# Optimization experiments

Hardware: AMD Instinct MI355X
Metric: run time of the kernel (lower is better)

The kernel has to match this reference:

```python
import jax, jax.numpy as jnp
import numpy as np

N = 100000
E = 1600000
F_IN = 512
H1, C1 = 8, 8          # conv1: 8 heads x 8 channels, concat -> 64
H2, C2 = 1, 16         # conv2: 1 head x num_classes=16, mean
NEG_SLOPE = 0.2


def setup_inputs() -> dict:
    key = jax.random.key(0)
    ks = jax.random.split(key, 10)
    x = jax.random.normal(ks[0], (N, F_IN), dtype=jnp.float32)
    edge_index = jax.random.randint(ks[1], (2, E), 0, N, dtype=jnp.int64)
    s1 = 1.0 / np.sqrt(F_IN)
    s2 = 1.0 / np.sqrt(H1 * C1)
    W1 = jax.random.normal(ks[2], (F_IN, H1 * C1), dtype=jnp.float32) * s1
    a1_src = jax.random.normal(ks[3], (H1, C1), dtype=jnp.float32) * 0.1
    a1_dst = jax.random.normal(ks[4], (H1, C1), dtype=jnp.float32) * 0.1
    b1 = jnp.zeros((H1 * C1,), dtype=jnp.float32)
    W2 = jax.random.normal(ks[5], (H1 * C1, H2 * C2), dtype=jnp.float32) * s2
    a2_src = jax.random.normal(ks[6], (H2, C2), dtype=jnp.float32) * 0.1
    a2_dst = jax.random.normal(ks[7], (H2, C2), dtype=jnp.float32) * 0.1
    b2 = jnp.zeros((C2,), dtype=jnp.float32)
    return {"x": x, "edge_index": edge_index, "W1": W1, "a1_src": a1_src,
            "a1_dst": a1_dst, "b1": b1, "W2": W2, "a2_src": a2_src,
            "a2_dst": a2_dst, "b2": b2}


def _add_self_loops(edge_index, n):
    loops = jnp.arange(n, dtype=edge_index.dtype)
    return jnp.concatenate([edge_index, jnp.stack([loops, loops])], axis=1)


def gat_conv(x, edge_index, W, a_src, a_dst, bias, concat):
    # x: [N, Fin]; W: [Fin, H*C]; a_*: [H, C]
    n = x.shape[0]
    H, C = a_src.shape
    h = (x @ W).reshape(n, H, C)                      # [N, H, C]
    al_src = jnp.einsum('nhc,hc->nh', h, a_src)       # [N, H]
    al_dst = jnp.einsum('nhc,hc->nh', h, a_dst)
    src, dst = edge_index[0], edge_index[1]
    e = al_src[src] + al_dst[dst]                     # [E, H]
    e = jnp.where(e > 0, e, NEG_SLOPE * e)            # LeakyReLU
    # segment softmax over destination nodes
    m = jax.ops.segment_max(e, dst, num_segments=n)   # [N, H]
    ex = jnp.exp(e - m[dst])
    s = jax.ops.segment_sum(ex, dst, num_segments=n)  # [N, H]
    alpha = ex / s[dst]                               # [E, H]
    msg = h[src] * alpha[:, :, None]                  # [E, H, C]
    out = jax.ops.segment_sum(msg, dst, num_segments=n)  # [N, H, C]
    if concat:
        out = out.reshape(n, H * C)
    else:
        out = out.mean(axis=1)
    return out + bias


def reference(x, edge_index, W1, a1_src, a1_dst, b1, W2, a2_src, a2_dst, b2):
    ei = _add_self_loops(edge_index, x.shape[0])
    h = gat_conv(x, ei, W1, a1_src, a1_dst, b1, concat=True)
    h = jax.nn.elu(h)
    h = gat_conv(h, ei, W2, a2_src, a2_dst, b2, concat=False)
    return jax.nn.log_softmax(h, axis=1)
```

## Files before the change

### kernel.cpp

```cpp
#include <hip/hip_runtime.h>
#include <math.h>

#define F_IN 512
#define NHEAD1 8
#define NC1 8
#define F1 64
#define NC2 16
#define NEG_SLOPE 0.2f
#define BSHIFT 7
#define PART_G 512
#define BUILD_CAP 4608

static __device__ __forceinline__ float leaky(float v) {
    return v > 0.0f ? v : NEG_SLOPE * v;
}

__global__ __launch_bounds__(256) void k_gemm1(const float* __restrict__ x,
                                               const float* __restrict__ W,
                                               const float* __restrict__ a1s,
                                               const float* __restrict__ a1d,
                                               float* __restrict__ h1,
                                               float* __restrict__ al1s,
                                               float* __restrict__ al1d, int N) {
    __shared__ float xs[32][68];
    __shared__ float wsm[32][64];
    const int tid = threadIdx.x;
    const int tx = tid & 15, ty = tid >> 4;
    const int row0 = blockIdx.x * 64;
    const int r = tid & 63;
    const int kq = tid >> 6;
    float acc[4][4] = {};

    for (int k0 = 0; k0 < F_IN; k0 += 32) {
        {
            int gr = row0 + r;
            float4 v0 = make_float4(0.f, 0.f, 0.f, 0.f), v1 = v0;
            if (gr < N) {
                const float* p = x + (size_t)gr * F_IN + k0 + kq * 8;
                v0 = *(const float4*)p;
                v1 = *(const float4*)(p + 4);
            }
            xs[kq * 8 + 0][r] = v0.x; xs[kq * 8 + 1][r] = v0.y;
            xs[kq * 8 + 2][r] = v0.z; xs[kq * 8 + 3][r] = v0.w;
            xs[kq * 8 + 4][r] = v1.x; xs[kq * 8 + 5][r] = v1.y;
            xs[kq * 8 + 6][r] = v1.z; xs[kq * 8 + 7][r] = v1.w;
            int wr = tid >> 4;
            int wc = (tid & 15) * 4;
            #pragma unroll
            for (int rr = 0; rr < 32; rr += 16) {
                *(float4*)(&wsm[wr + rr][wc]) =
                    *(const float4*)(W + (size_t)(k0 + wr + rr) * F1 + wc);
            }
        }
        __syncthreads();
        #pragma unroll
        for (int k = 0; k < 32; ++k) {
            float4 a = *(const float4*)(&xs[k][ty * 4]);
            float4 b = *(const float4*)(&wsm[k][tx * 4]);
            acc[0][0] = fmaf(a.x, b.x, acc[0][0]); acc[0][1] = fmaf(a.x, b.y, acc[0][1]);
            acc[0][2] = fmaf(a.x, b.z, acc[0][2]); acc[0][3] = fmaf(a.x, b.w, acc[0][3]);
            acc[1][0] = fmaf(a.y, b.x, acc[1][0]); acc[1][1] = fmaf(a.y, b.y, acc[1][1]);
            acc[1][2] = fmaf(a.y, b.z, acc[1][2]); acc[1][3] = fmaf(a.y, b.w, acc[1][3]);
            acc[2][0] = fmaf(a.z, b.x, acc[2][0]); acc[2][1] = fmaf(a.z, b.y, acc[2][1]);
            acc[2][2] = fmaf(a.z, b.z, acc[2][2]); acc[2][3] = fmaf(a.z, b.w, acc[2][3]);
            acc[3][0] = fmaf(a.w, b.x, acc[3][0]); acc[3][1] = fmaf(a.w, b.y, acc[3][1]);
            acc[3][2] = fmaf(a.w, b.z, acc[3][2]); acc[3][3] = fmaf(a.w, b.w, acc[3][3]);
        }
        __syncthreads();
    }
    const int h = tx >> 1;
    const float* as = a1s + h * 8 + (tx & 1) * 4;
    const float* ad = a1d + h * 8 + (tx & 1) * 4;
    float4 asv = *(const float4*)as;
    float4 adv = *(const float4*)ad;
    #pragma unroll
    for (int i = 0; i < 4; ++i) {
        int gr = row0 + ty * 4 + i;
        float ps = acc[i][0] * asv.x + acc[i][1] * asv.y
                 + acc[i][2] * asv.z + acc[i][3] * asv.w;
        float pd = acc[i][0] * adv.x + acc[i][1] * adv.y
                 + acc[i][2] * adv.z + acc[i][3] * adv.w;
        ps += __shfl_xor(ps, 1);
        pd += __shfl_xor(pd, 1);
        if (gr < N) {
            *(float4*)(h1 + (size_t)gr * F1 + tx * 4) =
                make_float4(acc[i][0], acc[i][1], acc[i][2], acc[i][3]);
            if ((tx & 1) == 0) {
                al1s[gr * 8 + h] = ps;
                al1d[gr * 8 + h] = pd;
            }
        }
    }
}

__global__ __launch_bounds__(256) void k_bcount(const int* __restrict__ ei,
                                                int* __restrict__ counts,
                                                int E, int NBUCK, int chunk) {
    __shared__ int cnt[1024];
    const int g = blockIdx.x, tid = threadIdx.x;
    for (int i = tid; i < NBUCK; i += 256) cnt[i] = 0;
    __syncthreads();
    int lo = g * chunk, hi = lo + chunk;
    if (hi > E) hi = E;
    for (int e = lo + tid; e < hi; e += 256)
        atomicAdd(&cnt[ei[E + e] >> BSHIFT], 1);
    __syncthreads();
    for (int k = tid; k < NBUCK; k += 256)
        counts[k * PART_G + g] = cnt[k];
}

__global__ __launch_bounds__(256) void k_scan_block(const int* __restrict__ in,
                                                    int* __restrict__ out,
                                                    int* __restrict__ blocksum, int L) {
    __shared__ int sdata[256];
    int t = threadIdx.x;
    int i = blockIdx.x * 256 + t;
    int v = (i < L) ? in[i] : 0;
    sdata[t] = v;
    __syncthreads();
    for (int off = 1; off < 256; off <<= 1) {
        int add = (t >= off) ? sdata[t - off] : 0;
        __syncthreads();
        sdata[t] += add;
        __syncthreads();
    }
    if (i < L) out[i] = sdata[t] - v;
    if (t == 255) blocksum[blockIdx.x] = sdata[t];
}

__global__ void k_scan_carry(const int* __restrict__ blocksum,
                             int* __restrict__ blockoffset, int NB) {
    int lane = threadIdx.x;
    int carry = 0;
    for (int base = 0; base < NB; base += 64) {
        int i = base + lane;
        int v = (i < NB) ? blocksum[i] : 0;
        int x = v;
        #pragma unroll
        for (int off = 1; off < 64; off <<= 1) {
            int y = __shfl_up(x, off);
            if (lane >= off) x += y;
        }
        if (i < NB) blockoffset[i] = carry + x - v;
        carry += __shfl(x, 63);
    }
}

__global__ void k_scan_addg(int* __restrict__ out, const int* __restrict__ boff, int L) {
    int i = blockIdx.x * blockDim.x + threadIdx.x;
    if (i < L) out[i] += boff[i >> 8];
}

__global__ __launch_bounds__(256) void k_bscatter(const int* __restrict__ ei,
                                                  const int* __restrict__ offs,
                                                  unsigned* __restrict__ packed,
                                                  int E, int NBUCK, int chunk) {
    __shared__ int cur[1024];
    const int g = blockIdx.x, tid = threadIdx.x;
    for (int k = tid; k < NBUCK; k += 256) cur[k] = offs[k * PART_G + g];
    __syncthreads();
    int lo = g * chunk, hi = lo + chunk;
    if (hi > E) hi = E;
    for (int e = lo + tid; e < hi; e += 256) {
        int src = ei[e], dst = ei[E + e];
        int pos = atomicAdd(&cur[dst >> BSHIFT], 1);
        packed[pos] = ((unsigned)(dst & 127) << 20) | (unsigned)src;
    }
}

__global__ __launch_bounds__(256) void k_bbuild(const unsigned* __restrict__ packed,
                                                const int* __restrict__ offs,
                                                int* __restrict__ rowptr,
                                                int* __restrict__ esrc,
                                                int E, int N, int NBUCK) {
    __shared__ int sdeg[128], sinc[128], scur[128];
    __shared__ int sbuf[BUILD_CAP];
    const int k = blockIdx.x, tid = threadIdx.x;
    const int s = offs[k * PART_G];
    const int e = (k + 1 < NBUCK) ? offs[(k + 1) * PART_G] : E;
    const int cnt = e - s;
    if (tid < 128) sdeg[tid] = 0;
    __syncthreads();
    for (int i = tid; i < cnt; i += 256)
        atomicAdd(&sdeg[packed[s + i] >> 20], 1);
    __syncthreads();
    if (tid < 128) sinc[tid] = sdeg[tid];
    __syncthreads();
    for (int off = 1; off < 128; off <<= 1) {
        int add = (tid < 128 && tid >= off) ? sinc[tid - off] : 0;
        __syncthreads();
        if (tid < 128) sinc[tid] += add;
        __syncthreads();
    }
    int nd = N - (k << BSHIFT);
    if (nd > 128) nd = 128;
    if (tid < nd) {
        int excl = sinc[tid] - sdeg[tid];
        rowptr[(k << BSHIFT) + tid] = s + excl;
        scur[tid] = excl;
    }
    if (k == 0 && tid == 0) rowptr[N] = E;
    __syncthreads();
    if (cnt <= BUILD_CAP) {
        for (int i = tid; i < cnt; i += 256) {
            unsigned p = packed[s + i];
            int pos = atomicAdd(&scur[p >> 20], 1);
            sbuf[pos] = (int)(p & 0xFFFFFu);
        }
        __syncthreads();
        for (int i = tid; i < cnt; i += 256) esrc[s + i] = sbuf[i];
    } else {
        for (int i = tid; i < cnt; i += 256) {
            unsigned p = packed[s + i];
            int pos = atomicAdd(&scur[p >> 20], 1);
            esrc[s + pos] = (int)(p & 0xFFFFFu);
        }
    }
}

__global__ __launch_bounds__(256) void k_agg1(
    const float* __restrict__ h1, const float* __restrict__ al1s,
    const float* __restrict__ al1d, const int* __restrict__ rowptr,
    const int* __restrict__ esrc, const float* __restrict__ b1,
    const float* __restrict__ W2, const float* __restrict__ a2s,
    const float* __restrict__ a2d, float* __restrict__ h2,
    float* __restrict__ al2s, float* __restrict__ al2d, int N) {
    const int lane = threadIdx.x & 63;
    const int wv = threadIdx.x >> 6;
    const int n = blockIdx.x * 4 + wv;
    const int h = lane >> 3;
    const int q = lane >> 4, c = lane & 15;
    if (n >= N) return;

    float w2reg[16];
    #pragma unroll
    for (int j = 0; j < 16; ++j) w2reg[j] = W2[(q * 16 + j) * NC2 + c];
    const float b1l = b1[lane];
    const float a2sc = a2s[c], a2dc = a2d[c];

    const float aldh = al1d[n * 8 + h];
    float w0 = __expf(leaky(al1s[n * 8 + h] + aldh));
    float s = w0;
    float acc = w0 * h1[(size_t)n * F1 + lane];

    const int start = rowptr[n], end = rowptr[n + 1];
    for (int base = start; base < end; base += 64) {
        int cntv = end - base;
        if (cntv > 64) cntv = 64;
        int msrc = (lane < cntv) ? esrc[base + lane] : 0;
        for (int j = 0; j < cntv; ++j) {
            int src = __shfl(msrc, j);
            float w = __expf(leaky(al1s[src * 8 + h] + aldh));
            float hv = h1[(size_t)src * F1 + lane];
            s += w;
            acc = fmaf(w, hv, acc);
        }
    }
    float v = acc / s + b1l;
    v = v > 0.0f ? v : expm1f(v);
    float part = 0.f;
    #pragma unroll
    for (int j = 0; j < 16; ++j)
        part += __shfl(v, q * 16 + j) * w2reg[j];
    part += __shfl_xor(part, 16);
    part += __shfl_xor(part, 32);
    float ts = part * a2sc, td = part * a2dc;
    #pragma unroll
    for (int off = 1; off < 16; off <<= 1) {
        ts += __shfl_xor(ts, off);
        td += __shfl_xor(td, off);
    }
    if (lane < 16) h2[(size_t)n * NC2 + c] = part;
    if (lane == 0) { al2s[n] = ts; al2d[n] = td; }
}

__global__ __launch_bounds__(256) void k_agg2(
    const float* __restrict__ h2, const float* __restrict__ al2s,
    const float* __restrict__ al2d, const int* __restrict__ rowptr,
    const int* __restrict__ esrc, const float* __restrict__ b2,
    float* __restrict__ out, int N) {
    const int lane = threadIdx.x & 63;
    const int wv = threadIdx.x >> 6;
    const int n = blockIdx.x * 4 + wv;
    const int q = lane >> 4, c = lane & 15;
    if (n >= N) return;
    const float b2c = b2[c];
    const float ald = al2d[n];
    float s, acc;
    if (q == 0) {
        float w0 = __expf(leaky(al2s[n] + ald));
        s = w0;
        acc = w0 * h2[(size_t)n * NC2 + c];
    } else {
        s = 0.f; acc = 0.f;
    }
    const int start = rowptr[n], end = rowptr[n + 1];
    for (int k = start + q; k < end; k += 4) {
        int src = esrc[k];
        float w = __expf(leaky(al2s[src] + ald));
        float hv = h2[(size_t)src * NC2 + c];
        s += w;
        acc = fmaf(w, hv, acc);
    }
    s += __shfl_xor(s, 16);   acc += __shfl_xor(acc, 16);
    s += __shfl_xor(s, 32);   acc += __shfl_xor(acc, 32);
    float v = acc / s + b2c;
    float mm = v;
    #pragma unroll
    for (int off = 1; off < 16; off <<= 1) mm = fmaxf(mm, __shfl_xor(mm, off));
    float se = __expf(v - mm);
    #pragma unroll
    for (int off = 1; off < 16; off <<= 1) se += __shfl_xor(se, off);
    if (lane < 16) out[(size_t)n * NC2 + c] = v - (logf(se) + mm);
}

extern "C" void kernel_launch(void* const* d_in, const int* in_sizes, int n_in,
                              void* d_out, int out_size, void* d_ws, size_t ws_size,
                              hipStream_t stream) {
    const float* x      = (const float*)d_in[0];
    const int*   ei     = (const int*)d_in[1];
    const float* W1     = (const float*)d_in[2];
    const float* a1_src = (const float*)d_in[3];
    const float* a1_dst = (const float*)d_in[4];
    const float* b1     = (const float*)d_in[5];
    const float* W2     = (const float*)d_in[6];
    const float* a2_src = (const float*)d_in[7];
    const float* a2_dst = (const float*)d_in[8];
    const float* b2     = (const float*)d_in[9];
    float* out = (float*)d_out;

    const int N = in_sizes[0] / F_IN;
    const int E = in_sizes[1] / 2;
    const int NH = N * NHEAD1;
    const int NBUCK = (N + 127) >> BSHIFT;
    const int L = NBUCK * PART_G;
    const int NB = (L + 255) / 256;
    const int chunk = (E + PART_G - 1) / PART_G;

    char* base = (char*)d_ws;
    size_t off = 0;
    auto alloc = [&](size_t bytes, size_t align) -> void* {
        off = (off + align - 1) & ~(align - 1);
        void* p = base + off; off += bytes; return p;
    };
    float* h1   = (float*)alloc((size_t)N * F1 * 4, 16);
    float* al1s = (float*)alloc((size_t)NH * 4, 16);
    float* al1d = (float*)alloc((size_t)NH * 4, 16);
    float* h2   = (float*)alloc((size_t)N * NC2 * 4, 16);
    float* al2s = (float*)alloc((size_t)N * 4, 16);
    float* al2d = (float*)alloc((size_t)N * 4, 16);
    int* rowptr = (int*)alloc((size_t)(N + 1) * 4, 16);
    int* esrc   = (int*)alloc((size_t)E * 4, 16);
    char* tbase = (char*)h1;
    unsigned* packed = (unsigned*)tbase;
    int* counts   = (int*)(tbase + (size_t)E * 4);
    int* offs     = counts + L;
    int* blocksum = offs + L;
    int* boffset  = blocksum + NB;

    const int B = 256;
    auto blocks = [](long long cnt, int b) { return (int)((cnt + b - 1) / b); };

    k_bcount<<<PART_G, 256, 0, stream>>>(ei, counts, E, NBUCK, chunk);
    k_scan_block<<<NB, 256, 0, stream>>>(counts, offs, blocksum, L);
    k_scan_carry<<<1, 64, 0, stream>>>(blocksum, boffset, NB);
    k_scan_addg<<<blocks(L, B), B, 0, stream>>>(offs, boffset, L);
    k_bscatter<<<PART_G, 256, 0, stream>>>(ei, offs, packed, E, NBUCK, chunk);
    k_bbuild<<<NBUCK, 256, 0, stream>>>(packed, offs, rowptr, esrc, E, N, NBUCK);

    k_gemm1<<<dim3((N + 63) / 64), dim3(256), 0, stream>>>(x, W1, a1_src, a1_dst,
                                                           h1, al1s, al1d, N);
    k_agg1<<<blocks(N, 4), 256, 0, stream>>>(h1, al1s, al1d, rowptr, esrc,
                                             b1, W2, a2_src, a2_dst,
                                             h2, al2s, al2d, N);
    k_agg2<<<blocks(N, 4), 256, 0, stream>>>(h2, al2s, al2d, rowptr, esrc, b2, out, N);
}
```

Before: 586.8 us.

## Process multiple edges per wave in GAT aggregations and fold scan carry-add into consumers

```diff
diff --git a/kernel.cpp b/kernel.cpp
--- a/kernel.cpp
+++ b/kernel.cpp
@@ -146,18 +146,17 @@
     }
 }
 
-__global__ void k_scan_addg(int* __restrict__ out, const int* __restrict__ boff, int L) {
-    int i = blockIdx.x * blockDim.x + threadIdx.x;
-    if (i < L) out[i] += boff[i >> 8];
-}
-
 __global__ __launch_bounds__(256) void k_bscatter(const int* __restrict__ ei,
                                                   const int* __restrict__ offs,
+                                                  const int* __restrict__ boff,
                                                   unsigned* __restrict__ packed,
                                                   int E, int NBUCK, int chunk) {
     __shared__ int cur[1024];
     const int g = blockIdx.x, tid = threadIdx.x;
-    for (int k = tid; k < NBUCK; k += 256) cur[k] = offs[k * PART_G + g];
+    for (int k = tid; k < NBUCK; k += 256) {
+        int idx = k * PART_G + g;
+        cur[k] = offs[idx] + boff[idx >> 8];
+    }
     __syncthreads();
     int lo = g * chunk, hi = lo + chunk;
     if (hi > E) hi = E;
@@ -170,14 +169,20 @@
 
 __global__ __launch_bounds__(256) void k_bbuild(const unsigned* __restrict__ packed,
                                                 const int* __restrict__ offs,
+                                                const int* __restrict__ boff,
                                                 int* __restrict__ rowptr,
                                                 int* __restrict__ esrc,
                                                 int E, int N, int NBUCK) {
     __shared__ int sdeg[128], sinc[128], scur[128];
     __shared__ int sbuf[BUILD_CAP];
     const int k = blockIdx.x, tid = threadIdx.x;
-    const int s = offs[k * PART_G];
-    const int e = (k + 1 < NBUCK) ? offs[(k + 1) * PART_G] : E;
+    const int i0 = k * PART_G;
+    const int s = offs[i0] + boff[i0 >> 8];
+    int e;
+    if (k + 1 < NBUCK) {
+        int i1 = (k + 1) * PART_G;
+        e = offs[i1] + boff[i1 >> 8];
+    } else e = E;
     const int cnt = e - s;
     if (tid < 128) sdeg[tid] = 0;
     __syncthreads();
@@ -228,49 +233,74 @@
     const int lane = threadIdx.x & 63;
     const int wv = threadIdx.x >> 6;
     const int n = blockIdx.x * 4 + wv;
-    const int h = lane >> 3;
-    const int q = lane >> 4, c = lane & 15;
     if (n >= N) return;
-
-    float w2reg[16];
-    #pragma unroll
-    for (int j = 0; j < 16; ++j) w2reg[j] = W2[(q * 16 + j) * NC2 + c];
-    const float b1l = b1[lane];
-    const float a2sc = a2s[c], a2dc = a2d[c];
+    const int sub = lane >> 4;
+    const int t = lane & 15;
+    const int h = t >> 1;
+
+    float4 w2r[4];
+    #pragma unroll
+    for (int j = 0; j < 4; ++j)
+        w2r[j] = *(const float4*)(W2 + (4 * t + j) * NC2 + 4 * sub);
+    const float4 b1v  = *(const float4*)(b1 + 4 * t);
+    const float4 a2sv = *(const float4*)(a2s + 4 * sub);
+    const float4 a2dv = *(const float4*)(a2d + 4 * sub);
 
     const float aldh = al1d[n * 8 + h];
-    float w0 = __expf(leaky(al1s[n * 8 + h] + aldh));
-    float s = w0;
-    float acc = w0 * h1[(size_t)n * F1 + lane];
-
+    float s = 0.f, acc0 = 0.f, acc1 = 0.f, acc2 = 0.f, acc3 = 0.f;
+    if (sub == 0) {
+        float w0 = __expf(leaky(al1s[n * 8 + h] + aldh));
+        float4 u = *(const float4*)(h1 + (size_t)n * F1 + t * 4);
+        s = w0;
+        acc0 = w0 * u.x; acc1 = w0 * u.y; acc2 = w0 * u.z; acc3 = w0 * u.w;
+    }
     const int start = rowptr[n], end = rowptr[n + 1];
     for (int base = start; base < end; base += 64) {
-        int cntv = end - base;
-        if (cntv > 64) cntv = 64;
-        int msrc = (lane < cntv) ? esrc[base + lane] : 0;
-        for (int j = 0; j < cntv; ++j) {
-            int src = __shfl(msrc, j);
-            float w = __expf(leaky(al1s[src * 8 + h] + aldh));
-            float hv = h1[(size_t)src * F1 + lane];
+        int cnt = end - base;
+        if (cnt > 64) cnt = 64;
+        int msrc = (lane < cnt) ? esrc[base + lane] : 0;
+        for (int j4 = 0; j4 < cnt; j4 += 4) {
+            int idx = j4 + sub;
+            int src = __shfl(msrc, idx);
+            float w = (idx < cnt) ? __expf(leaky(al1s[src * 8 + h] + aldh)) : 0.f;
+            float4 u = *(const float4*)(h1 + (size_t)src * F1 + t * 4);
             s += w;
-            acc = fmaf(w, hv, acc);
-        }
-    }
-    float v = acc / s + b1l;
-    v = v > 0.0f ? v : expm1f(v);
-    float part = 0.f;
-    #pragma unroll
-    for (int j = 0; j < 16; ++j)
-        part += __shfl(v, q * 16 + j) * w2reg[j];
-    part += __shfl_xor(part, 16);
-    part += __shfl_xor(part, 32);
-    float ts = part * a2sc, td = part * a2dc;
+            acc0 = fmaf(w, u.x, acc0);
+            acc1 = fmaf(w, u.y, acc1);
+            acc2 = fmaf(w, u.z, acc2);
+            acc3 = fmaf(w, u.w, acc3);
+        }
+    }
+    #pragma unroll
+    for (int off = 16; off < 64; off <<= 1) {
+        s    += __shfl_xor(s, off);
+        acc0 += __shfl_xor(acc0, off);
+        acc1 += __shfl_xor(acc1, off);
+        acc2 += __shfl_xor(acc2, off);
+        acc3 += __shfl_xor(acc3, off);
+    }
+    float rs = 1.0f / s;
+    float v0 = acc0 * rs + b1v.x; v0 = v0 > 0.f ? v0 : expm1f(v0);
+    float v1 = acc1 * rs + b1v.y; v1 = v1 > 0.f ? v1 : expm1f(v1);
+    float v2 = acc2 * rs + b1v.z; v2 = v2 > 0.f ? v2 : expm1f(v2);
+    float v3 = acc3 * rs + b1v.w; v3 = v3 > 0.f ? v3 : expm1f(v3);
+    float p0 = v0 * w2r[0].x + v1 * w2r[1].x + v2 * w2r[2].x + v3 * w2r[3].x;
+    float p1 = v0 * w2r[0].y + v1 * w2r[1].y + v2 * w2r[2].y + v3 * w2r[3].y;
+    float p2 = v0 * w2r[0].z + v1 * w2r[1].z + v2 * w2r[2].z + v3 * w2r[3].z;
+    float p3 = v0 * w2r[0].w + v1 * w2r[1].w + v2 * w2r[2].w + v3 * w2r[3].w;
     #pragma unroll
     for (int off = 1; off < 16; off <<= 1) {
-        ts += __shfl_xor(ts, off);
-        td += __shfl_xor(td, off);
-    }
-    if (lane < 16) h2[(size_t)n * NC2 + c] = part;
+        p0 += __shfl_xor(p0, off);
+        p1 += __shfl_xor(p1, off);
+        p2 += __shfl_xor(p2, off);
+        p3 += __shfl_xor(p3, off);
+    }
+    float ts = p0 * a2sv.x + p1 * a2sv.y + p2 * a2sv.z + p3 * a2sv.w;
+    float td = p0 * a2dv.x + p1 * a2dv.y + p2 * a2dv.z + p3 * a2dv.w;
+    ts += __shfl_xor(ts, 16); ts += __shfl_xor(ts, 32);
+    td += __shfl_xor(td, 16); td += __shfl_xor(td, 32);
+    if (t == 0)
+        *(float4*)(h2 + (size_t)n * NC2 + sub * 4) = make_float4(p0, p1, p2, p3);
     if (lane == 0) { al2s[n] = ts; al2d[n] = td; }
 }
 
@@ -282,36 +312,52 @@
     const int lane = threadIdx.x & 63;
     const int wv = threadIdx.x >> 6;
     const int n = blockIdx.x * 4 + wv;
-    const int q = lane >> 4, c = lane & 15;
     if (n >= N) return;
-    const float b2c = b2[c];
+    const int sub = lane >> 3;
+    const int t = lane & 7;
     const float ald = al2d[n];
-    float s, acc;
-    if (q == 0) {
+    float s = 0.f, a0 = 0.f, a1 = 0.f;
+    if (sub == 0) {
         float w0 = __expf(leaky(al2s[n] + ald));
+        float2 u = *(const float2*)(h2 + (size_t)n * NC2 + t * 2);
         s = w0;
-        acc = w0 * h2[(size_t)n * NC2 + c];
-    } else {
-        s = 0.f; acc = 0.f;
+        a0 = w0 * u.x;
+        a1 = w0 * u.y;
     }
     const int start = rowptr[n], end = rowptr[n + 1];
-    for (int k = start + q; k < end; k += 4) {
-        int src = esrc[k];
-        float w = __expf(leaky(al2s[src] + ald));
-        float hv = h2[(size_t)src * NC2 + c];
-        s += w;
-        acc = fmaf(w, hv, acc);
-    }
-    s += __shfl_xor(s, 16);   acc += __shfl_xor(acc, 16);
-    s += __shfl_xor(s, 32);   acc += __shfl_xor(acc, 32);
-    float v = acc / s + b2c;
-    float mm = v;
-    #pragma unroll
-    for (int off = 1; off < 16; off <<= 1) mm = fmaxf(mm, __shfl_xor(mm, off));
-    float se = __expf(v - mm);
-    #pragma unroll
-    for (int off = 1; off < 16; off <<= 1) se += __shfl_xor(se, off);
-    if (lane < 16) out[(size_t)n * NC2 + c] = v - (logf(se) + mm);
+    for (int base = start; base < end; base += 64) {
+        int cnt = end - base;
+        if (cnt > 64) cnt = 64;
+        int msrc = (lane < cnt) ? esrc[base + lane] : 0;
+        for (int j8 = 0; j8 < cnt; j8 += 8) {
+            int idx = j8 + sub;
+            int src = __shfl(msrc, idx);
+            float w = (idx < cnt) ? __expf(leaky(al2s[src] + ald)) : 0.f;
+            float2 u = *(const float2*)(h2 + (size_t)src * NC2 + t * 2);
+            s += w;
+            a0 = fmaf(w, u.x, a0);
+            a1 = fmaf(w, u.y, a1);
+        }
+    }
+    #pragma unroll
+    for (int off = 8; off < 64; off <<= 1) {
+        s  += __shfl_xor(s, off);
+        a0 += __shfl_xor(a0, off);
+        a1 += __shfl_xor(a1, off);
+    }
+    float rs = 1.0f / s;
+    float2 b2v = *(const float2*)(b2 + 2 * t);
+    float v0 = a0 * rs + b2v.x;
+    float v1 = a1 * rs + b2v.y;
+    float mm = fmaxf(v0, v1);
+    #pragma unroll
+    for (int off = 1; off < 8; off <<= 1) mm = fmaxf(mm, __shfl_xor(mm, off));
+    float se = __expf(v0 - mm) + __expf(v1 - mm);
+    #pragma unroll
+    for (int off = 1; off < 8; off <<= 1) se += __shfl_xor(se, off);
+    float l = logf(se) + mm;
+    if (sub == 0)
+        *(float2*)(out + (size_t)n * NC2 + 2 * t) = make_float2(v0 - l, v1 - l);
 }
 
 extern "C" void kernel_launch(void* const* d_in, const int* in_sizes, int n_in,
@@ -364,9 +410,8 @@
     k_bcount<<<PART_G, 256, 0, stream>>>(ei, counts, E, NBUCK, chunk);
     k_scan_block<<<NB, 256, 0, stream>>>(counts, offs, blocksum, L);
     k_scan_carry<<<1, 64, 0, stream>>>(blocksum, boffset, NB);
-    k_scan_addg<<<blocks(L, B), B, 0, stream>>>(offs, boffset, L);
-    k_bscatter<<<PART_G, 256, 0, stream>>>(ei, offs, packed, E, NBUCK, chunk);
-    k_bbuild<<<NBUCK, 256, 0, stream>>>(packed, offs, rowptr, esrc, E, N, NBUCK);
+    k_bscatter<<<PART_G, 256, 0, stream>>>(ei, offs, boffset, packed, E, NBUCK, chunk);
+    k_bbuild<<<NBUCK, 256, 0, stream>>>(packed, offs, boffset, rowptr, esrc, E, N, NBUCK);
 
     k_gemm1<<<dim3((N + 63) / 64), dim3(256), 0, stream>>>(x, W1, a1_src, a1_dst,
                                                            h1, al1s, al1d, N);
```

New measurement: 566.2 us. 3.5% less time.
